# Kernel tuning notes

Measured on AMD Instinct MI355X. Metric: run time of the kernel, lower is better.

## Reference

```python
import jax, jax.numpy as jnp
import numpy as np

N_SRC = 100000   # source nodes
N_DST = 100000   # destination nodes
E = 1600000      # edges (avg degree 16)
IN_F = 256       # in_features
HEADS = 8        # n_heads
OUT_F = 32       # out_features (per head)
HF = HEADS * OUT_F
NEG_SLOPE = 0.2  # standard GAT LeakyReLU slope


def setup_inputs() -> dict:
    key = jax.random.key(0)
    ks = jax.random.split(key, 8)
    sc = 0.05
    return {
        "x_src": jax.random.normal(ks[0], (N_SRC, IN_F), jnp.float32),
        "x_dst": jax.random.normal(ks[1], (N_DST, IN_F), jnp.float32),
        "Wv": jax.random.normal(ks[2], (IN_F, HF), jnp.float32) * sc,
        "bv": jnp.zeros((HF,), jnp.float32),
        "Wq": jax.random.normal(ks[3], (HF, HEADS), jnp.float32) * sc,
        "bq": jnp.zeros((HEADS,), jnp.float32),
        "Wk": jax.random.normal(ks[4], (HF, HEADS), jnp.float32) * sc,
        "bk": jnp.zeros((HEADS,), jnp.float32),
        "src_idx": jax.random.randint(ks[5], (E,), 0, N_SRC, dtype=jnp.int32),
        "dst_idx": jnp.sort(jax.random.randint(ks[6], (E,), 0, N_DST, dtype=jnp.int32)),
    }


def reference(x_src, x_dst, Wv, bv, Wq, bq, Wk, bk, src_idx, dst_idx):
    # dense projections (linear_v / linear_q / linear_k)
    h_src = x_src @ Wv + bv                       # [N_src, H*F]
    h_dst = x_dst @ Wv + bv                       # [N_dst, H*F]
    q = h_dst @ Wq + bq                           # [N_dst, H] per-head dst score
    k = h_src @ Wk + bk                           # [N_src, H] per-head src score

    # fused_gsddmm: edge score e = LeakyReLU(q[dst] + k[src]), then
    # softmax over incoming edges of each dst node (per head)
    e = jax.nn.leaky_relu(q[dst_idx] + k[src_idx], NEG_SLOPE)       # [E, H]
    m = jax.ops.segment_max(e, dst_idx, num_segments=N_DST)        # [N_dst, H]
    ex = jnp.exp(e - m[dst_idx])                                   # [E, H]
    s = jax.ops.segment_sum(ex, dst_idx, num_segments=N_DST)       # [N_dst, H]
    attn = ex / (s[dst_idx] + 1e-9)                                # [E, H]

    # gspmm: attention-weighted aggregation of src features to dst
    h_src3 = h_src.reshape(N_SRC, HEADS, OUT_F)                    # [N_src, H, F]
    msg = attn[:, :, None] * h_src3[src_idx]                       # [E, H, F]
    h = jax.ops.segment_sum(msg, dst_idx, num_segments=N_DST)      # [N_dst, H, F]

    return jnp.mean(h, axis=1)                                     # [N_dst, F]
```

## Files before the change

kernel.cpp:

```cpp
#include <hip/hip_runtime.h>
#include <hip/hip_bf16.h>
#include <stdint.h>

#define N_SRC_C 100000
#define N_DST_C 100000
#define M_TOT   200000
#define E_C     1600000
#define IN_FC   256
#define HEADS_C 8
#define OUT_FC  32
#define HF_C    256

#define BMg 128
#define BKg 32
#define BPITCH 40
#define A_ELEMS (BMg * BPITCH)
#define B_ROWS 272
#define B_ELEMS (B_ROWS * BPITCH)
#define B_CHUNKS 1360

typedef float f32x4_t __attribute__((ext_vector_type(4)));
typedef short s16x8_t __attribute__((ext_vector_type(8)));

static __device__ __forceinline__ unsigned short f2bf(float f) {
    union { __hip_bfloat16 h; unsigned short u; } cv;
    cv.h = __float2bfloat16(f);
    return cv.u;
}

static __device__ __forceinline__ s16x8_t cvt8(f32x4_t x0, f32x4_t x1) {
    union { s16x8_t v; unsigned short u[8]; } r;
    r.u[0] = f2bf(x0[0]); r.u[1] = f2bf(x0[1]);
    r.u[2] = f2bf(x0[2]); r.u[3] = f2bf(x0[3]);
    r.u[4] = f2bf(x1[0]); r.u[5] = f2bf(x1[1]);
    r.u[6] = f2bf(x1[2]); r.u[7] = f2bf(x1[3]);
    return r.v;
}

__global__ __launch_bounds__(256) void k_prep(
    const float* __restrict__ Wv, const float* __restrict__ bv,
    const float* __restrict__ Wq, const float* __restrict__ bq,
    const float* __restrict__ Wk, const float* __restrict__ bk,
    const int* __restrict__ dst_idx,
    unsigned short* __restrict__ WTpad, float* __restrict__ baux16,
    int* __restrict__ off) {
    const int b = blockIdx.x;
    const int tid = threadIdx.x;
    __shared__ float sq[4][8], sk[4][8];
    if (b < 257) {
        const int i = b;
        float vv = (i < 256) ? Wv[(size_t)i * HF_C + tid] : bv[tid];
        f32x4_t q0 = *(const f32x4_t*)(Wq + tid * 8);
        f32x4_t q1 = *(const f32x4_t*)(Wq + tid * 8 + 4);
        f32x4_t k0 = *(const f32x4_t*)(Wk + tid * 8);
        f32x4_t k1 = *(const f32x4_t*)(Wk + tid * 8 + 4);
        float pq[8], pk[8];
#pragma unroll
        for (int h = 0; h < 4; ++h) {
            pq[h] = vv * q0[h]; pq[4 + h] = vv * q1[h];
            pk[h] = vv * k0[h]; pk[4 + h] = vv * k1[h];
        }
#pragma unroll
        for (int m = 1; m < 64; m <<= 1) {
#pragma unroll
            for (int h = 0; h < 8; ++h) {
                pq[h] += __shfl_xor(pq[h], m);
                pk[h] += __shfl_xor(pk[h], m);
            }
        }
        const int w = tid >> 6, ln = tid & 63;
        if (ln == 0) {
#pragma unroll
            for (int h = 0; h < 8; ++h) { sq[w][h] = pq[h]; sk[w][h] = pk[h]; }
        }
        __syncthreads();
        if (tid < 8) {
            float fq = sq[0][tid] + sq[1][tid] + sq[2][tid] + sq[3][tid];
            float fk = sk[0][tid] + sk[1][tid] + sk[2][tid] + sk[3][tid];
            if (i < 256) {
                WTpad[(i >> 5) * B_ELEMS + (256 + tid) * BPITCH + (i & 31)] = f2bf(fk);
                WTpad[(i >> 5) * B_ELEMS + (264 + tid) * BPITCH + (i & 31)] = f2bf(fq);
            } else {
                baux16[tid]     = fk + bk[tid];
                baux16[8 + tid] = fq + bq[tid];
            }
        }
        if (i < 256)
            WTpad[(tid >> 5) * B_ELEMS + i * BPITCH + (tid & 31)] =
                f2bf(Wv[(size_t)tid * HF_C + i]);
    } else {
        int n = (b - 257) * 256 + tid;
        if (n > N_DST_C) return;
        if (n == N_DST_C) { off[n] = E_C; return; }
        int lo = 0, hi = E_C;
        while (lo < hi) {
            int mid = (lo + hi) >> 1;
            if (dst_idx[mid] < n) lo = mid + 1; else hi = mid;
        }
        off[n] = lo;
    }
}

__global__ __launch_bounds__(512, 4) void k_gemm(
    const float* __restrict__ Xs, const float* __restrict__ Xd,
    const unsigned short* __restrict__ WTpad,
    const float* __restrict__ bmain, const float* __restrict__ baux16,
    unsigned short* __restrict__ H, float* __restrict__ kko, float* __restrict__ qo) {
    __shared__ unsigned short smem[2 * A_ELEMS + 2 * B_ELEMS];
    unsigned short* As = smem;
    unsigned short* Bs = smem + 2 * A_ELEMS;
    const int tid  = threadIdx.x;
    const int lane = tid & 63;
    const int w    = tid >> 6;
    const int wr   = w >> 2, wc = w & 3;
    const int row0 = blockIdx.x * BMg;
    const bool need_main = (row0 < N_SRC_C);

    const int ar = tid >> 2, acg = tid & 3;
    int gr = row0 + ar; if (gr >= M_TOT) gr = M_TOT - 1;
    const float* arow = (gr < N_SRC_C) ? (Xs + (size_t)gr * IN_FC)
                                       : (Xd + (size_t)(gr - N_SRC_C) * IN_FC);

#define STAGE_B(kt, buf)                                                          \
    {                                                                             \
        const unsigned short* gsrc = WTpad + (size_t)(kt) * B_ELEMS;              \
        unsigned short* ldst = Bs + (buf) * B_ELEMS;                              \
        for (int g = w; g < 22; g += 8) {                                         \
            int c = g * 64 + lane;                                                \
            if (c < B_CHUNKS) {                                                   \
                __builtin_amdgcn_global_load_lds(                                 \
                    (const __attribute__((address_space(1))) unsigned int*)(gsrc + (size_t)c * 8), \
                    (__attribute__((address_space(3))) unsigned int*)(ldst + (size_t)c * 8),       \
                    16, 0, 0);                                                    \
            }                                                                     \
        }                                                                         \
    }

    f32x4_t acc[4][4];
    f32x4_t accA = {0.f, 0.f, 0.f, 0.f};
    const f32x4_t z = {0.f, 0.f, 0.f, 0.f};
#pragma unroll
    for (int m = 0; m < 4; ++m)
#pragma unroll
        for (int n = 0; n < 4; ++n) acc[m][n] = z;

    f32x4_t a0 = *(const f32x4_t*)(arow + acg * 8);
    f32x4_t a1 = *(const f32x4_t*)(arow + acg * 8 + 4);
    STAGE_B(0, 0);
    *(s16x8_t*)(As + ar * BPITCH + acg * 8) = cvt8(a0, a1);
    __syncthreads();
    a0 = *(const f32x4_t*)(arow + 32 + acg * 8);
    a1 = *(const f32x4_t*)(arow + 32 + acg * 8 + 4);
    STAGE_B(1, 1);

    const int koff = (lane >> 4) * 8;
    const int fr   = lane & 15;

    for (int kt = 0; kt < 8; ++kt) {
        const int cur = kt & 1;
        const unsigned short* Ab = As + cur * A_ELEMS;
        const unsigned short* Bb = Bs + cur * B_ELEMS;
        s16x8_t aa = *(const s16x8_t*)(Ab + (w * 16 + fr) * BPITCH + koff);
        s16x8_t ba = *(const s16x8_t*)(Bb + (256 + fr) * BPITCH + koff);
        accA = __builtin_amdgcn_mfma_f32_16x16x32_bf16(aa, ba, accA, 0, 0, 0);
        if (need_main) {
            s16x8_t a[4];
#pragma unroll
            for (int m = 0; m < 4; ++m)
                a[m] = *(const s16x8_t*)(Ab + (wr * 64 + m * 16 + fr) * BPITCH + koff);
#pragma unroll
            for (int n = 0; n < 4; ++n) {
                s16x8_t bf = *(const s16x8_t*)(Bb + (wc * 64 + n * 16 + fr) * BPITCH + koff);
#pragma unroll
                for (int m = 0; m < 4; ++m)
                    acc[m][n] = __builtin_amdgcn_mfma_f32_16x16x32_bf16(a[m], bf, acc[m][n], 0, 0, 0);
            }
        }
        if (kt < 7) {
            *(s16x8_t*)(As + (cur ^ 1) * A_ELEMS + ar * BPITCH + acg * 8) = cvt8(a0, a1);
            __syncthreads();
            if (kt < 6) {
                a0 = *(const f32x4_t*)(arow + (kt + 2) * 32 + acg * 8);
                a1 = *(const f32x4_t*)(arow + (kt + 2) * 32 + acg * 8 + 4);
                STAGE_B(kt + 2, cur);
            }
        }
    }

    {
        const int col0 = lane & 15;
        const float bb = baux16[col0];
        const int rb = row0 + w * 16 + (lane >> 4) * 4;
#pragma unroll
        for (int j = 0; j < 4; ++j) {
            int r = rb + j;
            float v = accA[j] + bb;
            if (r < N_SRC_C) {
                if (col0 < 8) kko[(size_t)r * 8 + col0] = v;
            } else if (r < M_TOT) {
                if (col0 >= 8) qo[(size_t)(r - N_SRC_C) * 8 + (col0 - 8)] = v;
            }
        }
    }

    if (need_main) {
        __syncthreads();
        unsigned short* reg = smem + w * 2304;
        float bb[4];
#pragma unroll
        for (int n = 0; n < 4; ++n) bb[n] = bmain[wc * 64 + n * 16 + fr];
#pragma unroll
        for (int g2 = 0; g2 < 2; ++g2) {
#pragma unroll
            for (int m2 = 0; m2 < 2; ++m2)
#pragma unroll
                for (int n = 0; n < 4; ++n)
#pragma unroll
                    for (int j = 0; j < 4; ++j) {
                        int lr = m2 * 16 + (lane >> 4) * 4 + j;
                        reg[lr * 72 + n * 16 + fr] = f2bf(acc[g2 * 2 + m2][n][j] + bb[n]);
                    }
#pragma unroll
            for (int i = 0; i < 4; ++i) {
                int lr = i * 8 + (lane >> 3);
                s16x8_t v = *(const s16x8_t*)(reg + lr * 72 + (lane & 7) * 8);
                int grr = row0 + wr * 64 + g2 * 32 + lr;
                if (grr < N_SRC_C)
                    *(s16x8_t*)(H + (size_t)grr * HF_C + wc * 64 + (lane & 7) * 8) = v;
            }
            __syncthreads();
        }
    }
#undef STAGE_B
}

__global__ __launch_bounds__(256) void k_edgew(
    const int* __restrict__ src_idx, const int* __restrict__ dst_idx,
    const float* __restrict__ q, const float* __restrict__ kk,
    float* __restrict__ w) {
    const int e = blockIdx.x * 256 + threadIdx.x;
    const int s = src_idx[e];
    const int d = dst_idx[e];
    f32x4_t q0 = *(const f32x4_t*)(q + (size_t)d * 8);
    f32x4_t q1 = *(const f32x4_t*)(q + (size_t)d * 8 + 4);
    f32x4_t k0 = *(const f32x4_t*)(kk + (size_t)s * 8);
    f32x4_t k1 = *(const f32x4_t*)(kk + (size_t)s * 8 + 4);
    f32x4_t w0, w1;
#pragma unroll
    for (int h = 0; h < 4; ++h) {
        float e0 = q0[h] + k0[h]; e0 = (e0 >= 0.f) ? e0 : 0.2f * e0;
        float e1 = q1[h] + k1[h]; e1 = (e1 >= 0.f) ? e1 : 0.2f * e1;
        w0[h] = __expf(e0);
        w1[h] = __expf(e1);
    }
    *(f32x4_t*)(w + (size_t)e * 8) = w0;
    *(f32x4_t*)(w + (size_t)e * 8 + 4) = w1;
}

__global__ __launch_bounds__(256) void k_gat_agg(
    const int* __restrict__ src_idx, const int* __restrict__ off,
    const float* __restrict__ w, const unsigned short* __restrict__ H,
    float* __restrict__ outp) {
    const int wv = (blockIdx.x * 256 + threadIdx.x) >> 6;
    const int lane = threadIdx.x & 63;
    if (wv >= N_DST_C) return;
    const int o0 = off[wv], o1 = off[wv + 1];
    const int e_sub = lane >> 3;
    const int h_w   = lane & 7;
    const int h_a   = lane >> 3;
    if (o1 <= o0) {
        if (lane < 8) {
            f32x4_t zv = {0.f, 0.f, 0.f, 0.f};
            *(f32x4_t*)(outp + (size_t)wv * 32 + lane * 4) = zv;
        }
        return;
    }
    const int last = o1 - 1;
    float den_w = 0.f;
    float a0 = 0.f, a1 = 0.f, a2 = 0.f, a3 = 0.f;
    const unsigned short* Hb = H + (size_t)h_a * 32 + (lane & 7) * 4;

    int s0 = src_idx[min(o0 + e_sub, last)];
    int s1 = src_idx[min(o0 + 8 + e_sub, last)];
    float w0 = w[(size_t)min(o0 + e_sub, last) * 8 + h_w];
    float w1 = w[(size_t)min(o0 + 8 + e_sub, last) * 8 + h_w];

    for (int base = o0; base < o1; base += 16) {
        const float p0 = (base + e_sub < o1) ? w0 : 0.f;
        const float p1 = (base + 8 + e_sub < o1) ? w1 : 0.f;
        den_w += p0 + p1;
        uint2 xa[8];
#pragma unroll
        for (int j = 0; j < 8; ++j) {
            const int se = __shfl(s0, j * 8);
            xa[j] = *(const uint2*)(Hb + (size_t)se * 256);
        }
        const int sn0 = src_idx[min(base + 16 + e_sub, last)];
        const int sn1 = src_idx[min(base + 24 + e_sub, last)];
        const float wn0 = w[(size_t)min(base + 16 + e_sub, last) * 8 + h_w];
        const float wn1 = w[(size_t)min(base + 24 + e_sub, last) * 8 + h_w];
#pragma unroll
        for (int j = 0; j < 8; ++j) {
            const float wgt = __shfl(p0, j * 8 + h_a);
            a0 += wgt * __uint_as_float(xa[j].x << 16);
            a1 += wgt * __uint_as_float(xa[j].x & 0xffff0000u);
            a2 += wgt * __uint_as_float(xa[j].y << 16);
            a3 += wgt * __uint_as_float(xa[j].y & 0xffff0000u);
        }
        uint2 xb[8];
#pragma unroll
        for (int j = 0; j < 8; ++j) {
            const int se = __shfl(s1, j * 8);
            xb[j] = *(const uint2*)(Hb + (size_t)se * 256);
        }
#pragma unroll
        for (int j = 0; j < 8; ++j) {
            const float wgt = __shfl(p1, j * 8 + h_a);
            a0 += wgt * __uint_as_float(xb[j].x << 16);
            a1 += wgt * __uint_as_float(xb[j].x & 0xffff0000u);
            a2 += wgt * __uint_as_float(xb[j].y << 16);
            a3 += wgt * __uint_as_float(xb[j].y & 0xffff0000u);
        }
        s0 = sn0; s1 = sn1; w0 = wn0; w1 = wn1;
    }
    den_w += __shfl_xor(den_w, 8);
    den_w += __shfl_xor(den_w, 16);
    den_w += __shfl_xor(den_w, 32);
    const float rs_w = 1.f / (den_w + 1e-9f);
    const float rs_a = __shfl(rs_w, h_a);
    a0 *= rs_a; a1 *= rs_a; a2 *= rs_a; a3 *= rs_a;
    a0 += __shfl_xor(a0, 8); a0 += __shfl_xor(a0, 16); a0 += __shfl_xor(a0, 32);
    a1 += __shfl_xor(a1, 8); a1 += __shfl_xor(a1, 16); a1 += __shfl_xor(a1, 32);
    a2 += __shfl_xor(a2, 8); a2 += __shfl_xor(a2, 16); a2 += __shfl_xor(a2, 32);
    a3 += __shfl_xor(a3, 8); a3 += __shfl_xor(a3, 16); a3 += __shfl_xor(a3, 32);
    if (lane < 8) {
        f32x4_t v = {a0 * 0.125f, a1 * 0.125f, a2 * 0.125f, a3 * 0.125f};
        *(f32x4_t*)(outp + (size_t)wv * 32 + lane * 4) = v;
    }
}

extern "C" void kernel_launch(void* const* d_in, const int* in_sizes, int n_in,
                              void* d_out, int out_size, void* d_ws, size_t ws_size,
                              hipStream_t stream) {
    const float* x_src = (const float*)d_in[0];
    const float* x_dst = (const float*)d_in[1];
    const float* Wv    = (const float*)d_in[2];
    const float* bv    = (const float*)d_in[3];
    const float* Wq    = (const float*)d_in[4];
    const float* bq    = (const float*)d_in[5];
    const float* Wk    = (const float*)d_in[6];
    const float* bk    = (const float*)d_in[7];
    const int* src_idx = (const int*)d_in[8];
    const int* dst_idx = (const int*)d_in[9];
    float* out = (float*)d_out;

    char* w = (char*)d_ws;
    unsigned short* H = (unsigned short*)w; w += (size_t)N_SRC_C * HF_C * 2;
    float* q  = (float*)w; w += (size_t)N_DST_C * HEADS_C * 4;
    float* kk = (float*)w; w += (size_t)N_SRC_C * HEADS_C * 4;
    float* ew = (float*)w; w += (size_t)E_C * HEADS_C * 4;
    int* off  = (int*)w;   w += 400128;
    unsigned short* WTpad = (unsigned short*)w; w += (size_t)8 * B_ELEMS * 2;
    float* baux16 = (float*)w; w += 256;

    k_prep<<<dim3(648), dim3(256), 0, stream>>>(Wv, bv, Wq, bq, Wk, bk, dst_idx,
                                                WTpad, baux16, off);
    k_gemm<<<dim3((M_TOT + BMg - 1) / BMg), dim3(512), 0, stream>>>(
        x_src, x_dst, WTpad, bv, baux16, H, kk, q);
    k_edgew<<<dim3(E_C / 256), dim3(256), 0, stream>>>(src_idx, dst_idx, q, kk, ew);
    k_gat_agg<<<dim3((N_DST_C + 3) / 4), dim3(256), 0, stream>>>(src_idx, off, ew, H, out);
}
```

Baseline: 218.7 us.

## Widen aggregation gathers to 16-byte loads and remap lanes to two edges per half-wave

Remaps the aggregation wavefront so each lane loads 8 bf16 features (uint4) rather than 4, with each half-wave handling a different edge. A full 256-feature row is now fetched by 32 lanes, so a 16-edge batch needs 8 wide gathers per lane instead of 16 narrow ones. All 16 loads are issued up front, before the weight prefetch, to improve memory-level parallelism. The cost is twice the accumulator registers and a reworked cross-lane reduction with more shuffles in the epilogue.

```diff
diff --git a/kernel.cpp b/kernel.cpp
--- a/kernel.cpp
+++ b/kernel.cpp
@@ -267,18 +267,23 @@
     const int o0 = off[wv], o1 = off[wv + 1];
     const int e_sub = lane >> 3;
     const int h_w   = lane & 7;
-    const int h_a   = lane >> 3;
+    const int hh    = (lane >> 2) & 7;
+    const int fc2   = lane & 3;
+    const int selA  = ((lane >> 5) << 3) | hh;
     if (o1 <= o0) {
-        if (lane < 8) {
+        if (lane < 4) {
             f32x4_t zv = {0.f, 0.f, 0.f, 0.f};
-            *(f32x4_t*)(outp + (size_t)wv * 32 + lane * 4) = zv;
+            *(f32x4_t*)(outp + (size_t)wv * 32 + lane * 8) = zv;
+            *(f32x4_t*)(outp + (size_t)wv * 32 + lane * 8 + 4) = zv;
         }
         return;
     }
     const int last = o1 - 1;
     float den_w = 0.f;
-    float a0 = 0.f, a1 = 0.f, a2 = 0.f, a3 = 0.f;
-    const unsigned short* Hb = H + (size_t)h_a * 32 + (lane & 7) * 4;
+    float a[8];
+#pragma unroll
+    for (int i = 0; i < 8; ++i) a[i] = 0.f;
+    const unsigned short* Hb = H + hh * 32 + fc2 * 8;
 
     int s0 = src_idx[min(o0 + e_sub, last)];
     int s1 = src_idx[min(o0 + 8 + e_sub, last)];
@@ -286,40 +291,35 @@
     float w1 = w[(size_t)min(o0 + 8 + e_sub, last) * 8 + h_w];
 
     for (int base = o0; base < o1; base += 16) {
+        uint4 xv[8];
+#pragma unroll
+        for (int j = 0; j < 4; ++j) {
+            const int se = __shfl(s0, j * 16 + selA);
+            xv[j] = *(const uint4*)(Hb + (size_t)se * 256);
+        }
+#pragma unroll
+        for (int j = 0; j < 4; ++j) {
+            const int se = __shfl(s1, j * 16 + selA);
+            xv[4 + j] = *(const uint4*)(Hb + (size_t)se * 256);
+        }
         const float p0 = (base + e_sub < o1) ? w0 : 0.f;
         const float p1 = (base + 8 + e_sub < o1) ? w1 : 0.f;
         den_w += p0 + p1;
-        uint2 xa[8];
-#pragma unroll
-        for (int j = 0; j < 8; ++j) {
-            const int se = __shfl(s0, j * 8);
-            xa[j] = *(const uint2*)(Hb + (size_t)se * 256);
-        }
         const int sn0 = src_idx[min(base + 16 + e_sub, last)];
         const int sn1 = src_idx[min(base + 24 + e_sub, last)];
         const float wn0 = w[(size_t)min(base + 16 + e_sub, last) * 8 + h_w];
         const float wn1 = w[(size_t)min(base + 24 + e_sub, last) * 8 + h_w];
 #pragma unroll
         for (int j = 0; j < 8; ++j) {
-            const float wgt = __shfl(p0, j * 8 + h_a);
-            a0 += wgt * __uint_as_float(xa[j].x << 16);
-            a1 += wgt * __uint_as_float(xa[j].x & 0xffff0000u);
-            a2 += wgt * __uint_as_float(xa[j].y << 16);
-            a3 += wgt * __uint_as_float(xa[j].y & 0xffff0000u);
-        }
-        uint2 xb[8];
-#pragma unroll
-        for (int j = 0; j < 8; ++j) {
-            const int se = __shfl(s1, j * 8);
-            xb[j] = *(const uint2*)(Hb + (size_t)se * 256);
-        }
-#pragma unroll
-        for (int j = 0; j < 8; ++j) {
-            const float wgt = __shfl(p1, j * 8 + h_a);
-            a0 += wgt * __uint_as_float(xb[j].x << 16);
-            a1 += wgt * __uint_as_float(xb[j].x & 0xffff0000u);
-            a2 += wgt * __uint_as_float(xb[j].y << 16);
-            a3 += wgt * __uint_as_float(xb[j].y & 0xffff0000u);
+            const float wgt = __shfl(j < 4 ? p0 : p1, (j & 3) * 16 + selA);
+            a[0] += wgt * __uint_as_float(xv[j].x << 16);
+            a[1] += wgt * __uint_as_float(xv[j].x & 0xffff0000u);
+            a[2] += wgt * __uint_as_float(xv[j].y << 16);
+            a[3] += wgt * __uint_as_float(xv[j].y & 0xffff0000u);
+            a[4] += wgt * __uint_as_float(xv[j].z << 16);
+            a[5] += wgt * __uint_as_float(xv[j].z & 0xffff0000u);
+            a[6] += wgt * __uint_as_float(xv[j].w << 16);
+            a[7] += wgt * __uint_as_float(xv[j].w & 0xffff0000u);
         }
         s0 = sn0; s1 = sn1; w0 = wn0; w1 = wn1;
     }
@@ -327,15 +327,20 @@
     den_w += __shfl_xor(den_w, 16);
     den_w += __shfl_xor(den_w, 32);
     const float rs_w = 1.f / (den_w + 1e-9f);
-    const float rs_a = __shfl(rs_w, h_a);
-    a0 *= rs_a; a1 *= rs_a; a2 *= rs_a; a3 *= rs_a;
-    a0 += __shfl_xor(a0, 8); a0 += __shfl_xor(a0, 16); a0 += __shfl_xor(a0, 32);
-    a1 += __shfl_xor(a1, 8); a1 += __shfl_xor(a1, 16); a1 += __shfl_xor(a1, 32);
-    a2 += __shfl_xor(a2, 8); a2 += __shfl_xor(a2, 16); a2 += __shfl_xor(a2, 32);
-    a3 += __shfl_xor(a3, 8); a3 += __shfl_xor(a3, 16); a3 += __shfl_xor(a3, 32);
-    if (lane < 8) {
-        f32x4_t v = {a0 * 0.125f, a1 * 0.125f, a2 * 0.125f, a3 * 0.125f};
-        *(f32x4_t*)(outp + (size_t)wv * 32 + lane * 4) = v;
+    const float rs_a = __shfl(rs_w, hh) * 0.125f;
+#pragma unroll
+    for (int i = 0; i < 8; ++i) {
+        a[i] += __shfl_xor(a[i], 32);
+        a[i] *= rs_a;
+        a[i] += __shfl_xor(a[i], 4);
+        a[i] += __shfl_xor(a[i], 8);
+        a[i] += __shfl_xor(a[i], 16);
+    }
+    if (lane < 4) {
+        f32x4_t v0 = {a[0], a[1], a[2], a[3]};
+        f32x4_t v1 = {a[4], a[5], a[6], a[7]};
+        *(f32x4_t*)(outp + (size_t)wv * 32 + lane * 8) = v0;
+        *(f32x4_t*)(outp + (size_t)wv * 32 + lane * 8 + 4) = v1;
     }
 }
 
```

Result: faster. 209.2 us (-4.3%).
